# Performance work log

Measured on AMD Instinct MI355X. Metric: run time of the kernel, lower is better.

## Reference

```python
import jax, jax.numpy as jnp
import numpy as np

V, E, H, B, S = 50257, 1024, 1024, 32, 1024

def setup_inputs() -> dict:
    key = jax.random.key(0)
    ks = jax.random.split(key, 16)
    s = 0.02
    return {
        "word_inputs": jax.random.randint(ks[0], (B, 1), 0, V),
        "hidden": jax.random.normal(ks[1], (1, B, H), jnp.float32),
        "output_encoder": jax.random.normal(ks[2], (B, S, H), jnp.float32),
        "emb": jax.random.normal(ks[3], (V, E), jnp.float32) * 0.2,
        "W_a1": jax.random.normal(ks[4], (H, 2 * H), jnp.float32) * s,
        "b_a1": jnp.zeros((H,), jnp.float32),
        "W_a2": jax.random.normal(ks[5], (1, H), jnp.float32) * s,
        "b_a2": jnp.zeros((1,), jnp.float32),
        "W_c": jax.random.normal(ks[6], (H, 2 * H), jnp.float32) * s,
        "b_c": jnp.zeros((H,), jnp.float32),
        "W_ih": jax.random.normal(ks[7], (3 * H, E), jnp.float32) * s,
        "W_hh": jax.random.normal(ks[8], (3 * H, H), jnp.float32) * s,
        "b_ih": jnp.zeros((3 * H,), jnp.float32),
        "b_hh": jnp.zeros((3 * H,), jnp.float32),
        "W_fc": jax.random.normal(ks[9], (V, H), jnp.float32) * 0.2,
        "b_fc": jnp.zeros((V,), jnp.float32),
    }

def reference(word_inputs, hidden, output_encoder, emb, W_a1, b_a1, W_a2, b_a2,
              W_c, b_c, W_ih, W_hh, b_ih, b_hh, W_fc, b_fc):
    b, s, h = output_encoder.shape
    h_prev = hidden[0]                                      # [B,H]
    # Bahdanau additive attention, vectorized over all S timesteps
    eh = jnp.concatenate(
        [output_encoder, jnp.broadcast_to(h_prev[:, None, :], (b, s, h))],
        axis=-1)                                            # [B,S,2H]
    scores = jnp.tanh(jnp.einsum('bsk,hk->bsh', eh, W_a1) + b_a1)
    scores = (jnp.einsum('bsh,oh->bso', scores, W_a2) + b_a2)[..., 0]  # [B,S]
    attn = jax.nn.softmax(scores, axis=1)                   # [B,S]
    context = jnp.einsum('bs,bsh->bh', attn, output_encoder)  # [B,H]
    embedded = emb[word_inputs.reshape(-1)]                 # [B,E]
    ec = jnp.concatenate([embedded, context], axis=-1)      # [B,E+H]
    x = jax.nn.relu(ec @ W_c.T + b_c)                       # [B,H]
    # single-step GRU (PyTorch gate order: r, z, n)
    gi = x @ W_ih.T + b_ih                                  # [B,3H]
    gh = h_prev @ W_hh.T + b_hh                             # [B,3H]
    i_r, i_z, i_n = jnp.split(gi, 3, axis=-1)
    h_r, h_z, h_n = jnp.split(gh, 3, axis=-1)
    r = jax.nn.sigmoid(i_r + h_r)
    z = jax.nn.sigmoid(i_z + h_z)
    n = jnp.tanh(i_n + r * h_n)
    h_new = (1.0 - z) * n + z * h_prev                      # [B,H]
    out = jax.nn.relu(h_new) @ W_fc.T + b_fc                # [B,V]
    return out, h_new[None, :, :]
```

## Files before the change

### kernel.cpp

```cpp
#include <hip/hip_runtime.h>

#define B_  32
#define S_  1024
#define H_  1024
#define V_  50257

typedef __attribute__((ext_vector_type(8))) short bf16x8;
typedef __attribute__((ext_vector_type(4))) float f32x4;
typedef __attribute__((ext_vector_type(8))) unsigned short u16x8;

__device__ __forceinline__ unsigned short f2b(float f) {
  union { float f; unsigned u; } v; v.f = f;
  unsigned r = 0x7FFFu + ((v.u >> 16) & 1u);
  return (unsigned short)((v.u + r) >> 16);
}
__device__ __forceinline__ float b2f(unsigned short h) {
  union { unsigned u; float f; } v; v.u = ((unsigned)h) << 16;
  return v.f;
}

__device__ __forceinline__ void async16(void* lds, const void* g) {
  typedef __attribute__((address_space(3))) void as3_void;
  typedef __attribute__((address_space(1))) void as1_void;
  as3_void* l = (as3_void*)(unsigned)(unsigned long long)lds;
  const as1_void* s = (const as1_void*)(unsigned long long)g;
  __builtin_amdgcn_global_load_lds(s, l, 16, 0, 0);
}

__global__ void conv_f32_bf16(const float* __restrict__ src, unsigned short* __restrict__ dst) {
  size_t i = ((size_t)blockIdx.x * 256 + threadIdx.x) * 8;
  float4 v0 = *(const float4*)(src + i);
  float4 v1 = *(const float4*)(src + i + 4);
  u16x8 o;
  o[0]=f2b(v0.x); o[1]=f2b(v0.y); o[2]=f2b(v0.z); o[3]=f2b(v0.w);
  o[4]=f2b(v1.x); o[5]=f2b(v1.y); o[6]=f2b(v1.z); o[7]=f2b(v1.w);
  *(u16x8*)(dst + i) = o;
}

__global__ void conv_wa1(const float* __restrict__ wa1, unsigned short* __restrict__ dst) {
  size_t i = ((size_t)blockIdx.x * 256 + threadIdx.x) * 8;
  int h = (int)(i >> 10), k = (int)(i & 1023);
  const float* s = wa1 + (size_t)h * 2048 + k;
  float4 v0 = *(const float4*)(s);
  float4 v1 = *(const float4*)(s + 4);
  u16x8 o;
  o[0]=f2b(v0.x); o[1]=f2b(v0.y); o[2]=f2b(v0.z); o[3]=f2b(v0.w);
  o[4]=f2b(v1.x); o[5]=f2b(v1.y); o[6]=f2b(v1.z); o[7]=f2b(v1.w);
  *(u16x8*)(dst + i) = o;
}

__global__ void part2_kernel(const float* __restrict__ wa1, const float* __restrict__ hidden,
                             const float* __restrict__ b_a1, float* __restrict__ part2) {
  int h = blockIdx.x;
  __shared__ float wrow[H_];
  for (int i = threadIdx.x; i < H_; i += 256) wrow[i] = wa1[(size_t)h * 2048 + 1024 + i];
  __syncthreads();
  int wave = threadIdx.x >> 6, lane = threadIdx.x & 63;
  float bias = b_a1[h];
  for (int bb = 0; bb < 8; ++bb) {
    int b = wave * 8 + bb;
    float acc = 0.f;
    for (int k = lane; k < H_; k += 64) acc += wrow[k] * hidden[b * H_ + k];
    #pragma unroll
    for (int off = 32; off; off >>= 1) acc += __shfl_xor(acc, off);
    if (lane == 0) part2[b * H_ + h] = acc + bias;
  }
}

__global__ __launch_bounds__(256) void scores_gemm(
    const unsigned short* __restrict__ A,
    const unsigned short* __restrict__ Bm,
    const float* __restrict__ part2,
    const float* __restrict__ wa2,
    float* __restrict__ partials)
{
  constexpr int K = H_;
  __shared__ __align__(16) unsigned short As[128 * 32];
  __shared__ __align__(16) unsigned short Bs[128 * 32];
  const int bm = blockIdx.x, bn = blockIdx.y;
  const int tid = threadIdx.x;
  const int wave = tid >> 6, lane = tid & 63;
  const int wr = wave >> 1, wc = wave & 1;
  const int l15 = lane & 15, l16 = lane >> 4;
  const int srow = lane >> 2, sseg = lane & 3;

  f32x4 acc[4][4];
  #pragma unroll
  for (int mi = 0; mi < 4; ++mi)
    #pragma unroll
    for (int ni = 0; ni < 4; ++ni) acc[mi][ni] = (f32x4){0.f, 0.f, 0.f, 0.f};

  for (int kt = 0; kt < K; kt += 32) {
    #pragma unroll
    for (int i = 0; i < 2; ++i) {
      int c = wave * 2 + i;
      int row = c * 16 + srow;
      async16(&As[c * 512], A  + (size_t)(bm * 128 + row) * K + kt + sseg * 8);
      async16(&Bs[c * 512], Bm + (size_t)(bn * 128 + row) * K + kt + sseg * 8);
    }
    asm volatile("s_waitcnt vmcnt(0)" ::: "memory");
    __syncthreads();
    bf16x8 af[4], bfr[4];
    #pragma unroll
    for (int mi = 0; mi < 4; ++mi)
      af[mi] = *(const bf16x8*)&As[(wr * 64 + mi * 16 + l15) * 32 + l16 * 8];
    #pragma unroll
    for (int ni = 0; ni < 4; ++ni)
      bfr[ni] = *(const bf16x8*)&Bs[(wc * 64 + ni * 16 + l15) * 32 + l16 * 8];
    #pragma unroll
    for (int mi = 0; mi < 4; ++mi)
      #pragma unroll
      for (int ni = 0; ni < 4; ++ni)
        acc[mi][ni] = __builtin_amdgcn_mfma_f32_16x16x32_bf16(af[mi], bfr[ni], acc[mi][ni], 0, 0, 0);
    __syncthreads();
  }

  const int b = bm >> 3;
  float w2[4], p2[4];
  #pragma unroll
  for (int ni = 0; ni < 4; ++ni) {
    int col = bn * 128 + wc * 64 + ni * 16 + l15;
    w2[ni] = wa2[col];
    p2[ni] = part2[b * H_ + col];
  }
  #pragma unroll
  for (int mi = 0; mi < 4; ++mi) {
    #pragma unroll
    for (int r = 0; r < 4; ++r) {
      float s = 0.f;
      #pragma unroll
      for (int ni = 0; ni < 4; ++ni)
        s += w2[ni] * tanhf(acc[mi][ni][r] + p2[ni]);
      s += __shfl_xor(s, 1); s += __shfl_xor(s, 2);
      s += __shfl_xor(s, 4); s += __shfl_xor(s, 8);
      if (l15 == 0) {
        int row = bm * 128 + wr * 64 + mi * 16 + l16 * 4 + r;
        partials[(size_t)row * 16 + bn * 2 + wc] = s;
      }
    }
  }
}

__global__ void softmax_kernel(const float* __restrict__ partials, const float* __restrict__ b_a2,
                               float* __restrict__ attn) {
  int b = blockIdx.x, s = threadIdx.x;
  int lane = s & 63, wid = s >> 6;
  const float4* p = (const float4*)(partials + (size_t)(b * S_ + s) * 16);
  float sc = b_a2[0];
  #pragma unroll
  for (int i = 0; i < 4; ++i) { float4 v = p[i]; sc += v.x + v.y + v.z + v.w; }
  __shared__ float rmax[16], rsum[16];
  float m = sc;
  #pragma unroll
  for (int off = 32; off; off >>= 1) m = fmaxf(m, __shfl_xor(m, off));
  if (lane == 0) rmax[wid] = m;
  __syncthreads();
  float M = rmax[0];
  #pragma unroll
  for (int i = 1; i < 16; ++i) M = fmaxf(M, rmax[i]);
  float e = expf(sc - M);
  float su = e;
  #pragma unroll
  for (int off = 32; off; off >>= 1) su += __shfl_xor(su, off);
  if (lane == 0) rsum[wid] = su;
  __syncthreads();
  float T = 0.f;
  #pragma unroll
  for (int i = 0; i < 16; ++i) T += rsum[i];
  attn[b * S_ + s] = e / T;
}

__global__ void ctx_partial_kernel(const unsigned short* __restrict__ encbf,
                                   const float* __restrict__ attn, float* __restrict__ ctxp) {
  int sc = blockIdx.x, b = blockIdx.y, t = threadIdx.x;
  int h4 = t * 4;
  float a0 = 0, a1 = 0, a2 = 0, a3 = 0;
  const unsigned short* base = encbf + (size_t)b * S_ * H_ + h4;
  const float* aw = attn + b * S_ + sc * 128;
  #pragma unroll 4
  for (int i = 0; i < 128; ++i) {
    float w = aw[i];
    ushort4 ev = *(const ushort4*)(base + (size_t)(sc * 128 + i) * H_);
    a0 += w * b2f(ev.x); a1 += w * b2f(ev.y); a2 += w * b2f(ev.z); a3 += w * b2f(ev.w);
  }
  float4 o = {a0, a1, a2, a3};
  *(float4*)(ctxp + (size_t)(sc * B_ + b) * H_ + h4) = o;
}

__global__ void prep_kernel(const float* __restrict__ ctxp, const float* __restrict__ emb,
                            const int* __restrict__ word, const float* __restrict__ hidden,
                            unsigned short* __restrict__ ec_bf, unsigned short* __restrict__ hprev_bf) {
  int b = blockIdx.x;
  int w = word[b];
  for (int h = threadIdx.x; h < H_; h += 256) {
    float c = 0.f;
    #pragma unroll
    for (int sc = 0; sc < 8; ++sc) c += ctxp[(size_t)(sc * B_ + b) * H_ + h];
    ec_bf[b * 2048 + 1024 + h] = f2b(c);
    ec_bf[b * 2048 + h] = f2b(emb[(size_t)w * H_ + h]);
    hprev_bf[b * H_ + h] = f2b(hidden[b * H_ + h]);
  }
}

__global__ __launch_bounds__(256) void skinny_gemm(
    const unsigned short* __restrict__ A, const float* __restrict__ Bw,
    float* __restrict__ C, const float* __restrict__ bias,
    int N, int K, int KC, int ldc, int mode)
{
  int n0 = blockIdx.x * 64;
  int kc = blockIdx.y;
  int wave = threadIdx.x >> 6, lane = threadIdx.x & 63;
  int l15 = lane & 15, l16 = lane >> 4;
  int col = n0 + wave * 16 + l15;
  int vclamp = col < N ? col : N - 1;
  const unsigned short* a0p = A + l15 * K + l16 * 8;
  const unsigned short* a1p = A + (16 + l15) * K + l16 * 8;
  const float* bp = Bw + (size_t)vclamp * K + l16 * 8;
  f32x4 acc0 = {0.f, 0.f, 0.f, 0.f}, acc1 = {0.f, 0.f, 0.f, 0.f};
  int k0 = kc * KC, k1 = (k0 + KC < K) ? (k0 + KC) : K;
  #pragma unroll 4
  for (int k = k0; k < k1; k += 32) {
    bf16x8 a0 = *(const bf16x8*)(a0p + k);
    bf16x8 a1 = *(const bf16x8*)(a1p + k);
    float4 bv0 = *(const float4*)(bp + k);
    float4 bv1 = *(const float4*)(bp + k + 4);
    bf16x8 bb;
    bb[0] = (short)f2b(bv0.x); bb[1] = (short)f2b(bv0.y);
    bb[2] = (short)f2b(bv0.z); bb[3] = (short)f2b(bv0.w);
    bb[4] = (short)f2b(bv1.x); bb[5] = (short)f2b(bv1.y);
    bb[6] = (short)f2b(bv1.z); bb[7] = (short)f2b(bv1.w);
    acc0 = __builtin_amdgcn_mfma_f32_16x16x32_bf16(a0, bb, acc0, 0, 0, 0);
    acc1 = __builtin_amdgcn_mfma_f32_16x16x32_bf16(a1, bb, acc1, 0, 0, 0);
  }
  if (col < N) {
    #pragma unroll
    for (int r = 0; r < 4; ++r) {
      int m = l16 * 4 + r;
      if (mode == 1) {
        float bv = bias[col];
        C[(size_t)m * ldc + col] = acc0[r] + bv;
        C[(size_t)(16 + m) * ldc + col] = acc1[r] + bv;
      } else {
        C[(size_t)(kc * 32 + m) * N + col] = acc0[r];
        C[(size_t)(kc * 32 + 16 + m) * N + col] = acc1[r];
      }
    }
  }
}

__global__ void xfinish_kernel(const float* __restrict__ xp, const float* __restrict__ b_c,
                               unsigned short* __restrict__ x_bf) {
  int i = blockIdx.x * 256 + threadIdx.x;
  int b = i >> 10, h = i & 1023;
  float v = b_c[h];
  #pragma unroll
  for (int kc = 0; kc < 8; ++kc) v += xp[(size_t)(kc * B_ + b) * H_ + h];
  x_bf[i] = f2b(v > 0.f ? v : 0.f);
}

__global__ void gates_kernel(const float* __restrict__ gip, const float* __restrict__ ghp,
                             const float* __restrict__ b_ih, const float* __restrict__ b_hh,
                             const float* __restrict__ hidden, float* __restrict__ hnew_out,
                             unsigned short* __restrict__ hr_bf) {
  int i = blockIdx.x * 256 + threadIdx.x;
  int b = i >> 10, h = i & 1023;
  float g[6];
  #pragma unroll
  for (int t = 0; t < 3; ++t) {
    int j = h + t * H_;
    float vi = b_ih[j], vh = b_hh[j];
    #pragma unroll
    for (int kc = 0; kc < 4; ++kc) {
      vi += gip[(size_t)(kc * B_ + b) * 3072 + j];
      vh += ghp[(size_t)(kc * B_ + b) * 3072 + j];
    }
    g[t] = vi; g[3 + t] = vh;
  }
  float r = 1.f / (1.f + expf(-(g[0] + g[3])));
  float z = 1.f / (1.f + expf(-(g[1] + g[4])));
  float n = tanhf(g[2] + r * g[5]);
  float hv = (1.f - z) * n + z * hidden[i];
  hnew_out[i] = hv;
  hr_bf[i] = f2b(hv > 0.f ? hv : 0.f);
}

extern "C" void kernel_launch(void* const* d_in, const int* in_sizes, int n_in,
                              void* d_out, int out_size, void* d_ws, size_t ws_size,
                              hipStream_t stream) {
  const int*   word   = (const int*)  d_in[0];
  const float* hidden = (const float*)d_in[1];
  const float* enc    = (const float*)d_in[2];
  const float* emb    = (const float*)d_in[3];
  const float* W_a1   = (const float*)d_in[4];
  const float* b_a1   = (const float*)d_in[5];
  const float* W_a2   = (const float*)d_in[6];
  const float* b_a2   = (const float*)d_in[7];
  const float* W_c    = (const float*)d_in[8];
  const float* b_c    = (const float*)d_in[9];
  const float* W_ih   = (const float*)d_in[10];
  const float* W_hh   = (const float*)d_in[11];
  const float* b_ih   = (const float*)d_in[12];
  const float* b_hh   = (const float*)d_in[13];
  const float* W_fc   = (const float*)d_in[14];
  const float* b_fc   = (const float*)d_in[15];
  float* out = (float*)d_out;

  if (ws_size < 77135872ull) return;

  char* ws = (char*)d_ws;
  unsigned short* enc_bf   = (unsigned short*)(ws + 0);
  unsigned short* wa1_bf   = (unsigned short*)(ws + 67108864);
  float*          part2    = (float*)         (ws + 69206016);
  float*          partials = (float*)         (ws + 69337088);
  float*          attn     = (float*)         (ws + 71434240);
  float*          ctxp     = (float*)         (ws + 71565312);
  unsigned short* ec_bf    = (unsigned short*)(ws + 72613888);
  unsigned short* hprev_bf = (unsigned short*)(ws + 72744960);
  float*          xp       = (float*)         (ws + 72810496);
  unsigned short* x_bf     = (unsigned short*)(ws + 73859072);
  float*          gip      = (float*)         (ws + 73924608);
  float*          ghp      = (float*)         (ws + 75497472);
  unsigned short* hr_bf    = (unsigned short*)(ws + 77070336);

  conv_f32_bf16<<<dim3(16384), dim3(256), 0, stream>>>(enc, enc_bf);
  conv_wa1<<<dim3(512), dim3(256), 0, stream>>>(W_a1, wa1_bf);
  part2_kernel<<<dim3(1024), dim3(256), 0, stream>>>(W_a1, hidden, b_a1, part2);
  scores_gemm<<<dim3(256, 8), dim3(256), 0, stream>>>(enc_bf, wa1_bf, part2, W_a2, partials);
  softmax_kernel<<<dim3(32), dim3(1024), 0, stream>>>(partials, b_a2, attn);
  ctx_partial_kernel<<<dim3(8, 32), dim3(256), 0, stream>>>(enc_bf, attn, ctxp);
  prep_kernel<<<dim3(32), dim3(256), 0, stream>>>(ctxp, emb, word, hidden, ec_bf, hprev_bf);
  skinny_gemm<<<dim3(16, 8), dim3(256), 0, stream>>>(ec_bf, W_c, xp, (const float*)nullptr,
                                                     1024, 2048, 256, 0, 0);
  xfinish_kernel<<<dim3(128), dim3(256), 0, stream>>>(xp, b_c, x_bf);
  skinny_gemm<<<dim3(48, 4), dim3(256), 0, stream>>>(x_bf, W_ih, gip, (const float*)nullptr,
                                                     3072, 1024, 256, 0, 0);
  skinny_gemm<<<dim3(48, 4), dim3(256), 0, stream>>>(hprev_bf, W_hh, ghp, (const float*)nullptr,
                                                     3072, 1024, 256, 0, 0);
  gates_kernel<<<dim3(128), dim3(256), 0, stream>>>(gip, ghp, b_ih, b_hh, hidden,
                                                    out + (size_t)B_ * V_, hr_bf);
  skinny_gemm<<<dim3(786, 1), dim3(256), 0, stream>>>(hr_bf, W_fc, out, b_fc,
                                                      V_, 1024, 1024, V_, 1);
}
```

Measured before the change: 305.8 us.

## Rewrite scores GEMM as 256x256 double-buffered pipelined tile; split-K other stages

Replaces the 128x128 single-buffered scores GEMM with a 512-thread, 256x256 tile kernel. It uses 128KB of dynamic LDS with double buffering, XOR swizzling, async prefetch two K-steps ahead, and interleaved MFMA phases with priority hints. The aim is to hide global-load latency and raise MFMA utilisation in the dominant GEMM. It also doubles split-K and sequence-chunk parallelism for the context and skinny GEMMs, and aliases workspace buffers. The cost is heavier register and LDS use and more partial sums to reduce.

```diff
diff --git a/kernel.cpp b/kernel.cpp
--- a/kernel.cpp
+++ b/kernel.cpp
@@ -67,64 +67,114 @@
   }
 }
 
-__global__ __launch_bounds__(256) void scores_gemm(
+#define NT_ 16
+#define BAR()  __builtin_amdgcn_s_barrier()
+#define SB0()  __builtin_amdgcn_sched_barrier(0)
+#define VM6()  asm volatile("s_waitcnt vmcnt(6)" ::: "memory")
+#define VM0()  asm volatile("s_waitcnt vmcnt(0)" ::: "memory")
+
+#define LOADA(MH) { _Pragma("unroll") for (int m_ = 0; m_ < 4; ++m_) \
+  { _Pragma("unroll") for (int ks_ = 0; ks_ < 2; ++ks_) { \
+    int r_ = wr*128 + (MH)*64 + m_*16 + l15; \
+    int lin_ = ks_*16384 + r_*64 + l16*16; \
+    int sw_ = lin_ ^ (((lin_>>9)&1)<<5); \
+    af[m_][ks_] = *(const bf16x8*)(smem + buf*32768 + sw_); } } }
+
+#define LOADB() { _Pragma("unroll") for (int n_ = 0; n_ < 4; ++n_) \
+  { _Pragma("unroll") for (int ks_ = 0; ks_ < 2; ++ks_) { \
+    int r_ = wc*64 + n_*16 + l15; \
+    int lin_ = ks_*16384 + r_*64 + l16*16; \
+    int sw_ = lin_ ^ (((lin_>>9)&1)<<5); \
+    bfr[n_][ks_] = *(const bf16x8*)(smem + 65536 + buf*32768 + sw_); } } }
+
+#define QUAD(MH, NH) { _Pragma("unroll") for (int m_ = 0; m_ < 4; ++m_) \
+  { _Pragma("unroll") for (int n_ = 0; n_ < 2; ++n_) { \
+    acc[(MH)*4+m_][(NH)*2+n_] = __builtin_amdgcn_mfma_f32_16x16x32_bf16(af[m_][0], bfr[(NH)*2+n_][0], acc[(MH)*4+m_][(NH)*2+n_], 0,0,0); \
+    acc[(MH)*4+m_][(NH)*2+n_] = __builtin_amdgcn_mfma_f32_16x16x32_bf16(af[m_][1], bfr[(NH)*2+n_][1], acc[(MH)*4+m_][(NH)*2+n_], 0,0,0); } } }
+
+#define PHASES(T, DO_B1, DO_T2, VMOP) { \
+  const int buf = (T) & 1; \
+  LOADA(0); LOADB(); \
+  if (DO_B1) stB((T)+1, 1, buf^1); \
+  BAR(); SB0(); \
+  __builtin_amdgcn_s_setprio(1); QUAD(0,0); __builtin_amdgcn_s_setprio(0); \
+  SB0(); BAR(); \
+  if (DO_T2) stB((T)+2, 0, buf); \
+  BAR(); SB0(); \
+  __builtin_amdgcn_s_setprio(1); QUAD(0,1); __builtin_amdgcn_s_setprio(0); \
+  SB0(); BAR(); \
+  LOADA(1); \
+  BAR(); SB0(); \
+  __builtin_amdgcn_s_setprio(1); QUAD(1,1); __builtin_amdgcn_s_setprio(0); \
+  SB0(); BAR(); \
+  if (DO_T2) { stA((T)+2, 0, buf); stA((T)+2, 1, buf); } \
+  VMOP; \
+  BAR(); SB0(); \
+  __builtin_amdgcn_s_setprio(1); QUAD(1,0); __builtin_amdgcn_s_setprio(0); \
+  SB0(); BAR(); }
+
+__global__ __launch_bounds__(512, 2) void scores_gemm8(
     const unsigned short* __restrict__ A,
     const unsigned short* __restrict__ Bm,
     const float* __restrict__ part2,
     const float* __restrict__ wa2,
     float* __restrict__ partials)
 {
-  constexpr int K = H_;
-  __shared__ __align__(16) unsigned short As[128 * 32];
-  __shared__ __align__(16) unsigned short Bs[128 * 32];
-  const int bm = blockIdx.x, bn = blockIdx.y;
+  extern __shared__ char smem[];
   const int tid = threadIdx.x;
   const int wave = tid >> 6, lane = tid & 63;
-  const int wr = wave >> 1, wc = wave & 1;
+  const int wr = wave >> 2, wc = wave & 3;
   const int l15 = lane & 15, l16 = lane >> 4;
-  const int srow = lane >> 2, sseg = lane & 3;
-
-  f32x4 acc[4][4];
-  #pragma unroll
-  for (int mi = 0; mi < 4; ++mi)
-    #pragma unroll
-    for (int ni = 0; ni < 4; ++ni) acc[mi][ni] = (f32x4){0.f, 0.f, 0.f, 0.f};
-
-  for (int kt = 0; kt < K; kt += 32) {
-    #pragma unroll
-    for (int i = 0; i < 2; ++i) {
-      int c = wave * 2 + i;
-      int row = c * 16 + srow;
-      async16(&As[c * 512], A  + (size_t)(bm * 128 + row) * K + kt + sseg * 8);
-      async16(&Bs[c * 512], Bm + (size_t)(bn * 128 + row) * K + kt + sseg * 8);
-    }
-    asm volatile("s_waitcnt vmcnt(0)" ::: "memory");
-    __syncthreads();
-    bf16x8 af[4], bfr[4];
-    #pragma unroll
-    for (int mi = 0; mi < 4; ++mi)
-      af[mi] = *(const bf16x8*)&As[(wr * 64 + mi * 16 + l15) * 32 + l16 * 8];
-    #pragma unroll
-    for (int ni = 0; ni < 4; ++ni)
-      bfr[ni] = *(const bf16x8*)&Bs[(wc * 64 + ni * 16 + l15) * 32 + l16 * 8];
-    #pragma unroll
-    for (int mi = 0; mi < 4; ++mi)
-      #pragma unroll
-      for (int ni = 0; ni < 4; ++ni)
-        acc[mi][ni] = __builtin_amdgcn_mfma_f32_16x16x32_bf16(af[mi], bfr[ni], acc[mi][ni], 0, 0, 0);
-    __syncthreads();
-  }
-
-  const int b = bm >> 3;
+  const int bm = blockIdx.x, bn = blockIdx.y;
+
+  const unsigned short* Abase = A  + (size_t)(bm * 256) * 1024;
+  const unsigned short* Bbase = Bm + (size_t)(bn * 256) * 1024;
+
+  const int Lc = tid * 16;
+  const int Ls = Lc ^ (((Lc >> 9) & 1) << 5);
+  const int sr = Ls >> 6;
+  const int sk = (Ls >> 1) & 31;
+
+  auto stA = [&](int t, int h, int db) {
+    char* base = smem + db * 32768 + h * 8192 + Lc;
+    const unsigned short* src = Abase + (size_t)(h * 128 + sr) * 1024 + t * 64 + sk;
+    async16(base,         src);
+    async16(base + 16384, src + 32);
+  };
+  auto stB = [&](int t, int h, int db) {
+    char* base = smem + 65536 + db * 32768 + h * 8192 + Lc;
+    const unsigned short* src = Bbase + (size_t)(h * 128 + sr) * 1024 + t * 64 + sk;
+    async16(base,         src);
+    async16(base + 16384, src + 32);
+  };
+
+  f32x4 acc[8][4];
+  #pragma unroll
+  for (int i = 0; i < 8; ++i)
+    #pragma unroll
+    for (int j = 0; j < 4; ++j) acc[i][j] = (f32x4){0.f, 0.f, 0.f, 0.f};
+  bf16x8 af[4][2], bfr[4][2];
+
+  stA(0, 0, 0); stA(0, 1, 0); stB(0, 0, 0); stB(0, 1, 0);
+  stB(1, 0, 1); stA(1, 0, 1); stA(1, 1, 1);
+  VM6();
+  BAR();
+
+  #pragma unroll 1
+  for (int t = 0; t < NT_ - 2; ++t) PHASES(t, 1, 1, VM6());
+  PHASES(NT_ - 2, 1, 0, VM0());
+  PHASES(NT_ - 1, 0, 0, (void)0);
+
+  const int b = bm >> 2;
   float w2[4], p2[4];
   #pragma unroll
   for (int ni = 0; ni < 4; ++ni) {
-    int col = bn * 128 + wc * 64 + ni * 16 + l15;
+    int col = bn * 256 + wc * 64 + ni * 16 + l15;
     w2[ni] = wa2[col];
     p2[ni] = part2[b * H_ + col];
   }
   #pragma unroll
-  for (int mi = 0; mi < 4; ++mi) {
+  for (int mi = 0; mi < 8; ++mi) {
     #pragma unroll
     for (int r = 0; r < 4; ++r) {
       float s = 0.f;
@@ -134,8 +184,8 @@
       s += __shfl_xor(s, 1); s += __shfl_xor(s, 2);
       s += __shfl_xor(s, 4); s += __shfl_xor(s, 8);
       if (l15 == 0) {
-        int row = bm * 128 + wr * 64 + mi * 16 + l16 * 4 + r;
-        partials[(size_t)row * 16 + bn * 2 + wc] = s;
+        int row = bm * 256 + wr * 128 + mi * 16 + l16 * 4 + r;
+        partials[(size_t)row * 16 + bn * 4 + wc] = s;
       }
     }
   }
@@ -176,11 +226,11 @@
   int h4 = t * 4;
   float a0 = 0, a1 = 0, a2 = 0, a3 = 0;
   const unsigned short* base = encbf + (size_t)b * S_ * H_ + h4;
-  const float* aw = attn + b * S_ + sc * 128;
+  const float* aw = attn + b * S_ + sc * 64;
   #pragma unroll 4
-  for (int i = 0; i < 128; ++i) {
+  for (int i = 0; i < 64; ++i) {
     float w = aw[i];
-    ushort4 ev = *(const ushort4*)(base + (size_t)(sc * 128 + i) * H_);
+    ushort4 ev = *(const ushort4*)(base + (size_t)(sc * 64 + i) * H_);
     a0 += w * b2f(ev.x); a1 += w * b2f(ev.y); a2 += w * b2f(ev.z); a3 += w * b2f(ev.w);
   }
   float4 o = {a0, a1, a2, a3};
@@ -195,7 +245,7 @@
   for (int h = threadIdx.x; h < H_; h += 256) {
     float c = 0.f;
     #pragma unroll
-    for (int sc = 0; sc < 8; ++sc) c += ctxp[(size_t)(sc * B_ + b) * H_ + h];
+    for (int sc = 0; sc < 16; ++sc) c += ctxp[(size_t)(sc * B_ + b) * H_ + h];
     ec_bf[b * 2048 + 1024 + h] = f2b(c);
     ec_bf[b * 2048 + h] = f2b(emb[(size_t)w * H_ + h]);
     hprev_bf[b * H_ + h] = f2b(hidden[b * H_ + h]);
@@ -254,7 +304,7 @@
   int b = i >> 10, h = i & 1023;
   float v = b_c[h];
   #pragma unroll
-  for (int kc = 0; kc < 8; ++kc) v += xp[(size_t)(kc * B_ + b) * H_ + h];
+  for (int kc = 0; kc < 16; ++kc) v += xp[(size_t)(kc * B_ + b) * H_ + h];
   x_bf[i] = f2b(v > 0.f ? v : 0.f);
 }
 
@@ -270,7 +320,7 @@
     int j = h + t * H_;
     float vi = b_ih[j], vh = b_hh[j];
     #pragma unroll
-    for (int kc = 0; kc < 4; ++kc) {
+    for (int kc = 0; kc < 8; ++kc) {
       vi += gip[(size_t)(kc * B_ + b) * 3072 + j];
       vh += ghp[(size_t)(kc * B_ + b) * 3072 + j];
     }
@@ -305,37 +355,40 @@
   const float* b_fc   = (const float*)d_in[15];
   float* out = (float*)d_out;
 
-  if (ws_size < 77135872ull) return;
+  if (ws_size < 71892992ull) return;
 
   char* ws = (char*)d_ws;
   unsigned short* enc_bf   = (unsigned short*)(ws + 0);
+  float*          gip      = (float*)         (ws + 0);
+  float*          ghp      = (float*)         (ws + 3145728);
   unsigned short* wa1_bf   = (unsigned short*)(ws + 67108864);
+  float*          xp       = (float*)         (ws + 67108864);
   float*          part2    = (float*)         (ws + 69206016);
   float*          partials = (float*)         (ws + 69337088);
+  float*          ctxp     = (float*)         (ws + 69337088);
   float*          attn     = (float*)         (ws + 71434240);
-  float*          ctxp     = (float*)         (ws + 71565312);
-  unsigned short* ec_bf    = (unsigned short*)(ws + 72613888);
-  unsigned short* hprev_bf = (unsigned short*)(ws + 72744960);
-  float*          xp       = (float*)         (ws + 72810496);
-  unsigned short* x_bf     = (unsigned short*)(ws + 73859072);
-  float*          gip      = (float*)         (ws + 73924608);
-  float*          ghp      = (float*)         (ws + 75497472);
-  unsigned short* hr_bf    = (unsigned short*)(ws + 77070336);
+  unsigned short* ec_bf    = (unsigned short*)(ws + 71565312);
+  unsigned short* hprev_bf = (unsigned short*)(ws + 71696384);
+  unsigned short* x_bf     = (unsigned short*)(ws + 71761920);
+  unsigned short* hr_bf    = (unsigned short*)(ws + 71827456);
+
+  hipFuncSetAttribute((const void*)scores_gemm8,
+                      hipFuncAttributeMaxDynamicSharedMemorySize, 131072);
 
   conv_f32_bf16<<<dim3(16384), dim3(256), 0, stream>>>(enc, enc_bf);
   conv_wa1<<<dim3(512), dim3(256), 0, stream>>>(W_a1, wa1_bf);
   part2_kernel<<<dim3(1024), dim3(256), 0, stream>>>(W_a1, hidden, b_a1, part2);
-  scores_gemm<<<dim3(256, 8), dim3(256), 0, stream>>>(enc_bf, wa1_bf, part2, W_a2, partials);
+  scores_gemm8<<<dim3(128, 4), dim3(512), 131072, stream>>>(enc_bf, wa1_bf, part2, W_a2, partials);
   softmax_kernel<<<dim3(32), dim3(1024), 0, stream>>>(partials, b_a2, attn);
-  ctx_partial_kernel<<<dim3(8, 32), dim3(256), 0, stream>>>(enc_bf, attn, ctxp);
+  ctx_partial_kernel<<<dim3(16, 32), dim3(256), 0, stream>>>(enc_bf, attn, ctxp);
   prep_kernel<<<dim3(32), dim3(256), 0, stream>>>(ctxp, emb, word, hidden, ec_bf, hprev_bf);
-  skinny_gemm<<<dim3(16, 8), dim3(256), 0, stream>>>(ec_bf, W_c, xp, (const float*)nullptr,
-                                                     1024, 2048, 256, 0, 0);
+  skinny_gemm<<<dim3(16, 16), dim3(256), 0, stream>>>(ec_bf, W_c, xp, (const float*)nullptr,
+                                                      1024, 2048, 128, 0, 0);
   xfinish_kernel<<<dim3(128), dim3(256), 0, stream>>>(xp, b_c, x_bf);
-  skinny_gemm<<<dim3(48, 4), dim3(256), 0, stream>>>(x_bf, W_ih, gip, (const float*)nullptr,
-                                                     3072, 1024, 256, 0, 0);
-  skinny_gemm<<<dim3(48, 4), dim3(256), 0, stream>>>(hprev_bf, W_hh, ghp, (const float*)nullptr,
-                                                     3072, 1024, 256, 0, 0);
+  skinny_gemm<<<dim3(48, 8), dim3(256), 0, stream>>>(x_bf, W_ih, gip, (const float*)nullptr,
+                                                     3072, 1024, 128, 0, 0);
+  skinny_gemm<<<dim3(48, 8), dim3(256), 0, stream>>>(hprev_bf, W_hh, ghp, (const float*)nullptr,
+                                                     3072, 1024, 128, 0, 0);
   gates_kernel<<<dim3(128), dim3(256), 0, stream>>>(gip, ghp, b_ih, b_hh, hidden,
                                                     out + (size_t)B_ * V_, hr_bf);
   skinny_gemm<<<dim3(786, 1), dim3(256), 0, stream>>>(hr_bf, W_fc, out, b_fc,
```

After: 291.3 us. -4.7%, faster.
